# Optimization experiments

Measured on AMD Instinct MI355X. Metric: run time of the kernel, lower is better.

## Reference

```python
import jax, jax.numpy as jnp
import numpy as np

EMBED = 768
NHEAD = 12
HEAD_DIM = EMBED // NHEAD


def setup_inputs() -> dict:
    key = jax.random.key(0)
    ks = jax.random.split(key, 6)
    bs, seq = 4, 2048
    x = jax.random.normal(ks[0], (bs, seq, EMBED), dtype=jnp.float32)
    attmask = jax.random.randint(ks[1], (bs, seq), 0, 2, dtype=jnp.int32)
    # xavier-uniform-ish init for weights
    lim_qkv = float(np.sqrt(6.0 / (EMBED + 3 * EMBED)))
    W_qkv = jax.random.uniform(ks[2], (EMBED, 3 * EMBED), minval=-lim_qkv, maxval=lim_qkv, dtype=jnp.float32)
    b_qkv = jnp.zeros((3 * EMBED,), dtype=jnp.float32)
    lim_p = float(np.sqrt(6.0 / (EMBED + EMBED)))
    W_proj = jax.random.uniform(ks[3], (EMBED, EMBED), minval=-lim_p, maxval=lim_p, dtype=jnp.float32)
    b_proj = jnp.zeros((EMBED,), dtype=jnp.float32)
    return {"x": x, "attmask": attmask, "W_qkv": W_qkv, "b_qkv": b_qkv, "W_proj": W_proj, "b_proj": b_proj}


def reference(x, attmask, W_qkv, b_qkv, W_proj, b_proj):
    bs, seq, embed = x.shape
    qkv = x @ W_qkv + b_qkv                     # [bs, seq, 3*embed]
    q, k, v = jnp.split(qkv, 3, axis=-1)
    def to_heads(t):
        return t.reshape(bs, seq, NHEAD, HEAD_DIM).transpose(0, 2, 1, 3)  # [bs, h, seq, d]
    q, k, v = to_heads(q), to_heads(k), to_heads(v)
    scale = 1.0 / np.sqrt(HEAD_DIM).astype(np.float32)
    scores = jnp.einsum('bhqd,bhkd->bhqk', q, k) * scale  # [bs, h, seq, seq]
    mask = (attmask == 0)[:, None, None, :]               # [bs,1,1,seq]
    scores = jnp.where(mask, jnp.asarray(-10000.0, scores.dtype), scores)
    att = jax.nn.softmax(scores, axis=-1)                  # dropout p=0.0 -> identity
    y = jnp.einsum('bhqk,bhkd->bhqd', att, v)              # [bs, h, seq, d]
    y = y.transpose(0, 2, 1, 3).reshape(bs, seq, embed)
    return y @ W_proj + b_proj
```

## Files before the change

kernel.cpp:

```cpp
#include <hip/hip_runtime.h>

typedef unsigned short u16;
typedef unsigned int u32;
typedef __attribute__((ext_vector_type(8))) short short8;
typedef __attribute__((ext_vector_type(4))) short s16x4;
typedef __attribute__((ext_vector_type(4))) float f32x4;

__device__ __forceinline__ float b2f(u16 u) {
    union { u32 i; float f; } v; v.i = ((u32)u) << 16; return v.f;
}
__device__ __forceinline__ u16 f2b(float f) {
    union { u32 i; float f; } v; v.f = f;
    u32 u = v.i;
    return (u16)((u + 0x7FFFu + ((u >> 16) & 1u)) >> 16);
}
__device__ __forceinline__ f32x4 zero4() {
    f32x4 v; v[0] = 0.f; v[1] = 0.f; v[2] = 0.f; v[3] = 0.f; return v;
}
__device__ __forceinline__ u32 cvtpk(float lo, float hi) {
    u32 d;
    asm("v_cvt_pk_bf16_f32 %0, %1, %2" : "=v"(d) : "v"(lo), "v"(hi));
    return d;
}
__device__ __forceinline__ float fexp2(float x) {
#if __has_builtin(__builtin_amdgcn_exp2f)
    return __builtin_amdgcn_exp2f(x);
#else
    return __expf(x * 0.6931471805599453f);
#endif
}
__device__ __forceinline__ void gload16(const u16* g, u16* l) {
    __builtin_amdgcn_global_load_lds(
        (const __attribute__((address_space(1))) u32*)g,
        (__attribute__((address_space(3))) u32*)l, 16, 0, 0);
}

__device__ __forceinline__ void tconv_body(const float* __restrict__ src,
                                           u16* __restrict__ dst,
                                           int K, int N, int bx, int by) {
    __shared__ u16 T[64][72];
    const int n0 = bx * 64, k0 = by * 64;
    const int tid = threadIdx.x;
    const int r = tid >> 3, cq = tid & 7;
#pragma unroll
    for (int half = 0; half < 2; half++) {
        const int k = k0 + half * 32 + r;
        const float* s = &src[(size_t)k * N + n0 + cq * 8];
        const float4 f0 = ((const float4*)s)[0];
        const float4 f1 = ((const float4*)s)[1];
        T[cq * 8 + 0][half * 32 + r] = f2b(f0.x);
        T[cq * 8 + 1][half * 32 + r] = f2b(f0.y);
        T[cq * 8 + 2][half * 32 + r] = f2b(f0.z);
        T[cq * 8 + 3][half * 32 + r] = f2b(f0.w);
        T[cq * 8 + 4][half * 32 + r] = f2b(f1.x);
        T[cq * 8 + 5][half * 32 + r] = f2b(f1.y);
        T[cq * 8 + 6][half * 32 + r] = f2b(f1.z);
        T[cq * 8 + 7][half * 32 + r] = f2b(f1.w);
    }
    __syncthreads();
#pragma unroll
    for (int half = 0; half < 2; half++) {
        const int n = half * 32 + r;
        short8 o = *(const short8*)&T[n][cq * 8];
        *(short8*)&dst[(size_t)(n0 + n) * K + k0 + cq * 8] = o;
    }
}

__global__ void prep_kernel(const float* __restrict__ x, u16* __restrict__ xb,
                            const float* __restrict__ Wqkv, u16* __restrict__ Wqkvb,
                            const float* __restrict__ Wproj, u16* __restrict__ Wprojb,
                            int n8x) {
    const int blk = blockIdx.x;
    if (blk < 432) {
        tconv_body(Wqkv, Wqkvb, 768, 2304, blk % 36, blk / 36);
    } else if (blk < 576) {
        const int id = blk - 432;
        tconv_body(Wproj, Wprojb, 768, 768, id % 12, id / 12);
    } else {
        const int stride = (1152 - 576) * 256;
        for (int i = (blk - 576) * 256 + threadIdx.x; i < n8x; i += stride) {
            const float* s = x + (size_t)i * 8;
            float4 a = ((const float4*)s)[0];
            float4 b = ((const float4*)s)[1];
            short8 o;
            o[0] = (short)f2b(a.x); o[1] = (short)f2b(a.y);
            o[2] = (short)f2b(a.z); o[3] = (short)f2b(a.w);
            o[4] = (short)f2b(b.x); o[5] = (short)f2b(b.y);
            o[6] = (short)f2b(b.z); o[7] = (short)f2b(b.w);
            ((short8*)xb)[i] = o;
        }
    }
}

template <int MODE>
__global__ __launch_bounds__(256, 2) void gemm_bt_kernel(
    const u16* __restrict__ A, const u16* __restrict__ Bt,
    const float* __restrict__ bias,
    u16* __restrict__ O0, u16* __restrict__ O1, u16* __restrict__ O2,
    float* __restrict__ Of,
    int M, int N, int K)
{
    __shared__ u16 As[128 * 64];
    __shared__ u16 Bs[128 * 64];

    const int tid = threadIdx.x;
    const int nwgx = gridDim.x;
    const int nwg = nwgx * gridDim.y;
    int lin = blockIdx.y * nwgx + blockIdx.x;
    lin = (lin & 7) * (nwg >> 3) + (lin >> 3);
    const int m0 = (lin / nwgx) * 128, n0 = (lin % nwgx) * 128;
    const int lane = tid & 63, w = tid >> 6;
    const int quad = lane >> 4, c = lane & 15;
    const int wm = (w & 1) * 64, wn = (w >> 1) * 64;

    f32x4 acc[4][4];
#pragma unroll
    for (int i = 0; i < 4; i++)
#pragma unroll
        for (int j = 0; j < 4; j++) acc[i][j] = zero4();

    const int srow = lane >> 3;
    const int scol = ((lane & 7) ^ ((srow & 1) << 2)) * 8;
    const size_t abase = (size_t)(m0 + w * 32 + srow) * K + scol;
    const size_t bbase = (size_t)(n0 + w * 32 + srow) * K + scol;
    u16* asl = &As[w * 32 * 64];
    u16* bsl = &Bs[w * 32 * 64];

    const int cpar = (c & 1) << 2;

    for (int k0 = 0; k0 < K; k0 += 64) {
        __syncthreads();
#pragma unroll
        for (int i = 0; i < 4; i++)
            gload16(A + abase + (size_t)(i * 8) * K + k0, asl + i * 512);
#pragma unroll
        for (int i = 0; i < 4; i++)
            gload16(Bt + bbase + (size_t)(i * 8) * K + k0, bsl + i * 512);
        asm volatile("s_waitcnt vmcnt(0)" ::: "memory");
        __syncthreads();

        short8 af[4][2], bfr[4][2];
#pragma unroll
        for (int mi = 0; mi < 4; mi++)
#pragma unroll
            for (int kk = 0; kk < 2; kk++)
                af[mi][kk] = *(const short8*)
                    &As[(wm + mi * 16 + c) * 64 + (((kk * 4 + quad) ^ cpar) * 8)];
#pragma unroll
        for (int ni = 0; ni < 4; ni++)
#pragma unroll
            for (int kk = 0; kk < 2; kk++)
                bfr[ni][kk] = *(const short8*)
                    &Bs[(wn + ni * 16 + c) * 64 + (((kk * 4 + quad) ^ cpar) * 8)];
#pragma unroll
        for (int kk = 0; kk < 2; kk++)
#pragma unroll
            for (int mi = 0; mi < 4; mi++)
#pragma unroll
                for (int ni = 0; ni < 4; ni++)
                    acc[mi][ni] = __builtin_amdgcn_mfma_f32_16x16x32_bf16(
                        af[mi][kk], bfr[ni][kk], acc[mi][ni], 0, 0, 0);
    }

#pragma unroll
    for (int ni = 0; ni < 4; ni++) {
        const int gc = n0 + wn + ni * 16 + c;
        const float bv = bias[gc];
        if (MODE == 0) {
            const int which = gc / 768;
            const int e = gc - which * 768;
            const int hh = e >> 6, d = e & 63;
            u16* op = (which == 0) ? O0 : (which == 1 ? O1 : O2);
#pragma unroll
            for (int mi = 0; mi < 4; mi++)
#pragma unroll
                for (int r = 0; r < 4; r++) {
                    const int gr = m0 + wm + mi * 16 + quad * 4 + r;
                    const int bb = gr >> 11, s = gr & 2047;
                    op[(((size_t)bb * 12 + hh) * 2048 + s) * 64 + d] =
                        f2b(acc[mi][ni][r] + bv);
                }
        } else {
#pragma unroll
            for (int mi = 0; mi < 4; mi++)
#pragma unroll
                for (int r = 0; r < 4; r++) {
                    const int gr = m0 + wm + mi * 16 + quad * 4 + r;
                    Of[(size_t)gr * N + gc] = acc[mi][ni][r] + bv;
                }
        }
    }
}

__global__ __launch_bounds__(256, 3) void attn_kernel(
    const u16* __restrict__ Q, const u16* __restrict__ Kv,
    const u16* __restrict__ Vv, const int* __restrict__ attmask,
    u16* __restrict__ Y)
{
    const int S = 2048, D = 64, NH = 12;
    __shared__ u16 Ks[64][72];
    __shared__ u16 Vs[64][68];
    __shared__ u16 Ps[4][2][16][72];
    __shared__ float msf[2048];

    const int tid = threadIdx.x;
    const int w = tid >> 6, lane = tid & 63;
    const int quad = lane >> 4, c = lane & 15;
    const int bh = blockIdx.x;
    const int qt = blockIdx.y;
    const int b = bh / NH, h = bh - b * NH;

    const u16* Qh = Q + (size_t)bh * S * D;
    const u16* Kh = Kv + (size_t)bh * S * D;
    const u16* Vh = Vv + (size_t)bh * S * D;
    const int q0 = qt * 128 + w * 16;

    short8 aq00 = *(const short8*)&Qh[(size_t)(q0 + c) * D + quad * 8];
    short8 aq01 = *(const short8*)&Qh[(size_t)(q0 + c) * D + 32 + quad * 8];
    short8 aq10 = *(const short8*)&Qh[(size_t)(q0 + 64 + c) * D + quad * 8];
    short8 aq11 = *(const short8*)&Qh[(size_t)(q0 + 64 + c) * D + 32 + quad * 8];

    for (int i = tid; i < S; i += 256)
        msf[i] = (attmask[b * S + i] == 0) ? -43282.0f : 0.0f;

    f32x4 o_acc[2][4];
#pragma unroll
    for (int g = 0; g < 2; g++)
#pragma unroll
        for (int i = 0; i < 4; i++) o_acc[g][i] = zero4();
    float l0 = 0.f, l1 = 0.f;

    const int kpos = tid >> 2, kd = (tid & 3) * 8;
    const int p2 = tid >> 3, vd = (tid & 7) * 8;

    short8 k0r = *(const short8*)&Kh[(size_t)kpos * D + kd];
    short8 k1r = *(const short8*)&Kh[(size_t)kpos * D + kd + 32];
    short8 v0r = *(const short8*)&Vh[(size_t)(2 * p2) * D + vd];
    short8 v1r = *(const short8*)&Vh[(size_t)(2 * p2 + 1) * D + vd];

    const float SC = 0.18033688f;

    for (int kt = 0; kt < S / 64; kt++) {
        asm volatile("" ::: "memory");
        __builtin_amdgcn_s_barrier();
        asm volatile("" ::: "memory");
        *(short8*)&Ks[kpos][kd] = k0r;
        *(short8*)&Ks[kpos][kd + 32] = k1r;
#pragma unroll
        for (int j = 0; j < 8; j++) {
            u32 pk = (u32)(u16)v0r[j] | ((u32)(u16)v1r[j] << 16);
            *(u32*)&Vs[vd + j][2 * p2] = pk;
        }
        if (kt + 1 < S / 64) {
            const int nb = (kt + 1) * 64;
            k0r = *(const short8*)&Kh[(size_t)(nb + kpos) * D + kd];
            k1r = *(const short8*)&Kh[(size_t)(nb + kpos) * D + kd + 32];
            v0r = *(const short8*)&Vh[(size_t)(nb + 2 * p2) * D + vd];
            v1r = *(const short8*)&Vh[(size_t)(nb + 2 * p2 + 1) * D + vd];
        }
        asm volatile("s_waitcnt lgkmcnt(0)" ::: "memory");
        __builtin_amdgcn_s_barrier();
        asm volatile("" ::: "memory");

        const int kbase = kt * 64;

        f32x4 s0[4], s1[4];
#pragma unroll
        for (int ni = 0; ni < 4; ni++) { s0[ni] = zero4(); s1[ni] = zero4(); }
        __builtin_amdgcn_s_setprio(1);
#pragma unroll
        for (int ni = 0; ni < 4; ni++) {
            short8 bk0 = *(const short8*)&Ks[ni * 16 + c][quad * 8];
            short8 bk1 = *(const short8*)&Ks[ni * 16 + c][32 + quad * 8];
            s0[ni] = __builtin_amdgcn_mfma_f32_16x16x32_bf16(bk0, aq00, s0[ni], 0, 0, 0);
            s0[ni] = __builtin_amdgcn_mfma_f32_16x16x32_bf16(bk1, aq01, s0[ni], 0, 0, 0);
            s1[ni] = __builtin_amdgcn_mfma_f32_16x16x32_bf16(bk0, aq10, s1[ni], 0, 0, 0);
            s1[ni] = __builtin_amdgcn_mfma_f32_16x16x32_bf16(bk1, aq11, s1[ni], 0, 0, 0);
        }
        __builtin_amdgcn_s_setprio(0);

#pragma unroll
        for (int ni = 0; ni < 4; ni++) {
            const f32x4 bias = *(const f32x4*)&msf[kbase + ni * 16 + quad * 4];
            {
                float p0 = fexp2(fmaf(s0[ni][0], SC, bias[0]));
                float p1 = fexp2(fmaf(s0[ni][1], SC, bias[1]));
                float p2f = fexp2(fmaf(s0[ni][2], SC, bias[2]));
                float p3 = fexp2(fmaf(s0[ni][3], SC, bias[3]));
                l0 += (p0 + p1) + (p2f + p3);
                uint2 pk;
                pk.x = cvtpk(p0, p1);
                pk.y = cvtpk(p2f, p3);
                *(uint2*)&Ps[w][0][c][ni * 16 + quad * 4] = pk;
            }
            {
                float p0 = fexp2(fmaf(s1[ni][0], SC, bias[0]));
                float p1 = fexp2(fmaf(s1[ni][1], SC, bias[1]));
                float p2f = fexp2(fmaf(s1[ni][2], SC, bias[2]));
                float p3 = fexp2(fmaf(s1[ni][3], SC, bias[3]));
                l1 += (p0 + p1) + (p2f + p3);
                uint2 pk;
                pk.x = cvtpk(p0, p1);
                pk.y = cvtpk(p2f, p3);
                *(uint2*)&Ps[w][1][c][ni * 16 + quad * 4] = pk;
            }
        }

        short8 ap00 = *(const short8*)&Ps[w][0][c][quad * 8];
        short8 ap01 = *(const short8*)&Ps[w][0][c][32 + quad * 8];
        short8 ap10 = *(const short8*)&Ps[w][1][c][quad * 8];
        short8 ap11 = *(const short8*)&Ps[w][1][c][32 + quad * 8];
        __builtin_amdgcn_s_setprio(1);
#pragma unroll
        for (int ni = 0; ni < 4; ni++) {
            union { short8 v8; s16x4 v4[2]; } u0, u1;
            u0.v4[0] = *(const s16x4*)&Vs[ni * 16 + c][quad * 8];
            u0.v4[1] = *(const s16x4*)&Vs[ni * 16 + c][quad * 8 + 4];
            u1.v4[0] = *(const s16x4*)&Vs[ni * 16 + c][32 + quad * 8];
            u1.v4[1] = *(const s16x4*)&Vs[ni * 16 + c][32 + quad * 8 + 4];
            o_acc[0][ni] = __builtin_amdgcn_mfma_f32_16x16x32_bf16(ap00, u0.v8, o_acc[0][ni], 0, 0, 0);
            o_acc[0][ni] = __builtin_amdgcn_mfma_f32_16x16x32_bf16(ap01, u1.v8, o_acc[0][ni], 0, 0, 0);
            o_acc[1][ni] = __builtin_amdgcn_mfma_f32_16x16x32_bf16(ap10, u0.v8, o_acc[1][ni], 0, 0, 0);
            o_acc[1][ni] = __builtin_amdgcn_mfma_f32_16x16x32_bf16(ap11, u1.v8, o_acc[1][ni], 0, 0, 0);
        }
        __builtin_amdgcn_s_setprio(0);
    }

    l0 += __shfl_xor(l0, 16);
    l0 += __shfl_xor(l0, 32);
    l1 += __shfl_xor(l1, 16);
    l1 += __shfl_xor(l1, 32);

    const size_t ybase = ((size_t)b * S) * 768 + h * 64;
#pragma unroll
    for (int r = 0; r < 4; r++) {
        const float lr0 = __shfl(l0, quad * 4 + r);
        const float lr1 = __shfl(l1, quad * 4 + r);
        const float inv0 = 1.f / fmaxf(lr0, 1e-30f);
        const float inv1 = 1.f / fmaxf(lr1, 1e-30f);
        const int srow0 = qt * 128 + w * 16 + quad * 4 + r;
        const int srow1 = srow0 + 64;
#pragma unroll
        for (int ni = 0; ni < 4; ni++) {
            Y[ybase + (size_t)srow0 * 768 + ni * 16 + c] = f2b(o_acc[0][ni][r] * inv0);
            Y[ybase + (size_t)srow1 * 768 + ni * 16 + c] = f2b(o_acc[1][ni][r] * inv1);
        }
    }
}

extern "C" void kernel_launch(void* const* d_in, const int* in_sizes, int n_in,
                              void* d_out, int out_size, void* d_ws, size_t ws_size,
                              hipStream_t stream) {
    const float* x     = (const float*)d_in[0];
    const int* attmask = (const int*)d_in[1];
    const float* Wqkv  = (const float*)d_in[2];
    const float* bqkv  = (const float*)d_in[3];
    const float* Wproj = (const float*)d_in[4];
    const float* bproj = (const float*)d_in[5];
    float* outf = (float*)d_out;

    u16* base = (u16*)d_ws;
    const size_t nx = 4ull * 2048 * 768;
    const size_t nwqkv = 768ull * 2304;
    const size_t nwproj = 768ull * 768;
    u16* xb     = base;
    u16* Wqkvb  = xb + nx;
    u16* Wprojb = Wqkvb + nwqkv;
    u16* Qb     = Wprojb + nwproj;
    const size_t headElems = 48ull * 2048 * 64;
    u16* Kb = Qb + headElems;
    u16* Vb = Kb + headElems;
    u16* Yb = Vb + headElems;

    prep_kernel<<<1152, 256, 0, stream>>>(x, xb, Wqkv, Wqkvb, Wproj, Wprojb,
                                          (int)(nx / 8));

    gemm_bt_kernel<0><<<dim3(18, 64), 256, 0, stream>>>(
        xb, Wqkvb, bqkv, Qb, Kb, Vb, nullptr, 8192, 2304, 768);
    attn_kernel<<<dim3(48, 16), 256, 0, stream>>>(Qb, Kb, Vb, attmask, Yb);
    gemm_bt_kernel<1><<<dim3(6, 64), 256, 0, stream>>>(
        Yb, Wprojb, bproj, nullptr, nullptr, nullptr, outf, 8192, 768, 768);
}
```

Measured before the change: 227.8 us.

## Double-buffer GEMM LDS tiles and vectorize epilogue via swapped MFMA operands

The projection GEMM kernel gets two LDS buffers per operand, so the next K tile is prefetched while MFMAs run on the current one, with a partial vmcnt wait and raw barriers. The MFMA operand order is swapped so each lane holds four consecutive output columns, which lets the epilogue pack bf16 pairs and issue 8-byte (QKV) or 16-byte (fp32) stores with a vector bias load instead of scalar stores. The cost is doubled LDS use, 64 KB per block, which may limit occupancy under launch_bounds(256,2).

```diff
diff --git a/kernel.cpp b/kernel.cpp
--- a/kernel.cpp
+++ b/kernel.cpp
@@ -100,8 +100,8 @@
     float* __restrict__ Of,
     int M, int N, int K)
 {
-    __shared__ u16 As[128 * 64];
-    __shared__ u16 Bs[128 * 64];
+    __shared__ u16 As[2][128 * 64];
+    __shared__ u16 Bs[2][128 * 64];
 
     const int tid = threadIdx.x;
     const int nwgx = gridDim.x;
@@ -123,21 +123,42 @@
     const int scol = ((lane & 7) ^ ((srow & 1) << 2)) * 8;
     const size_t abase = (size_t)(m0 + w * 32 + srow) * K + scol;
     const size_t bbase = (size_t)(n0 + w * 32 + srow) * K + scol;
-    u16* asl = &As[w * 32 * 64];
-    u16* bsl = &Bs[w * 32 * 64];
 
     const int cpar = (c & 1) << 2;
 
-    for (int k0 = 0; k0 < K; k0 += 64) {
-        __syncthreads();
+    {
+        u16* asl = &As[0][w * 2048];
+        u16* bsl = &Bs[0][w * 2048];
 #pragma unroll
         for (int i = 0; i < 4; i++)
-            gload16(A + abase + (size_t)(i * 8) * K + k0, asl + i * 512);
+            gload16(A + abase + (size_t)(i * 8) * K, asl + i * 512);
 #pragma unroll
         for (int i = 0; i < 4; i++)
-            gload16(Bt + bbase + (size_t)(i * 8) * K + k0, bsl + i * 512);
-        asm volatile("s_waitcnt vmcnt(0)" ::: "memory");
-        __syncthreads();
+            gload16(Bt + bbase + (size_t)(i * 8) * K, bsl + i * 512);
+    }
+
+    const int niter = K >> 6;
+    int cur = 0;
+    for (int it = 0; it < niter; it++) {
+        asm volatile("" ::: "memory");
+        __builtin_amdgcn_s_barrier();
+        asm volatile("" ::: "memory");
+        if (it + 1 < niter) {
+            const size_t k1 = (size_t)(it + 1) * 64;
+            u16* asl = &As[cur ^ 1][w * 2048];
+            u16* bsl = &Bs[cur ^ 1][w * 2048];
+#pragma unroll
+            for (int i = 0; i < 4; i++)
+                gload16(A + abase + (size_t)(i * 8) * K + k1, asl + i * 512);
+#pragma unroll
+            for (int i = 0; i < 4; i++)
+                gload16(Bt + bbase + (size_t)(i * 8) * K + k1, bsl + i * 512);
+            asm volatile("s_waitcnt vmcnt(8)" ::: "memory");
+        } else {
+            asm volatile("s_waitcnt vmcnt(0)" ::: "memory");
+        }
+        __builtin_amdgcn_s_barrier();
+        asm volatile("" ::: "memory");
 
         short8 af[4][2], bfr[4][2];
 #pragma unroll
@@ -145,13 +166,13 @@
 #pragma unroll
             for (int kk = 0; kk < 2; kk++)
                 af[mi][kk] = *(const short8*)
-                    &As[(wm + mi * 16 + c) * 64 + (((kk * 4 + quad) ^ cpar) * 8)];
+                    &As[cur][(wm + mi * 16 + c) * 64 + (((kk * 4 + quad) ^ cpar) * 8)];
 #pragma unroll
         for (int ni = 0; ni < 4; ni++)
 #pragma unroll
             for (int kk = 0; kk < 2; kk++)
                 bfr[ni][kk] = *(const short8*)
-                    &Bs[(wn + ni * 16 + c) * 64 + (((kk * 4 + quad) ^ cpar) * 8)];
+                    &Bs[cur][(wn + ni * 16 + c) * 64 + (((kk * 4 + quad) ^ cpar) * 8)];
 #pragma unroll
         for (int kk = 0; kk < 2; kk++)
 #pragma unroll
@@ -159,35 +180,39 @@
 #pragma unroll
                 for (int ni = 0; ni < 4; ni++)
                     acc[mi][ni] = __builtin_amdgcn_mfma_f32_16x16x32_bf16(
-                        af[mi][kk], bfr[ni][kk], acc[mi][ni], 0, 0, 0);
+                        bfr[ni][kk], af[mi][kk], acc[mi][ni], 0, 0, 0);
+        cur ^= 1;
     }
 
 #pragma unroll
     for (int ni = 0; ni < 4; ni++) {
-        const int gc = n0 + wn + ni * 16 + c;
-        const float bv = bias[gc];
+        const int gcb = n0 + wn + ni * 16 + quad * 4;
+        const f32x4 bv = *(const f32x4*)&bias[gcb];
         if (MODE == 0) {
-            const int which = gc / 768;
-            const int e = gc - which * 768;
+            const int which = gcb / 768;
+            const int e = gcb - which * 768;
             const int hh = e >> 6, d = e & 63;
             u16* op = (which == 0) ? O0 : (which == 1 ? O1 : O2);
 #pragma unroll
-            for (int mi = 0; mi < 4; mi++)
-#pragma unroll
-                for (int r = 0; r < 4; r++) {
-                    const int gr = m0 + wm + mi * 16 + quad * 4 + r;
-                    const int bb = gr >> 11, s = gr & 2047;
-                    op[(((size_t)bb * 12 + hh) * 2048 + s) * 64 + d] =
-                        f2b(acc[mi][ni][r] + bv);
-                }
+            for (int mi = 0; mi < 4; mi++) {
+                const int gr = m0 + wm + mi * 16 + c;
+                const int bb = gr >> 11, s = gr & 2047;
+                uint2 pk;
+                pk.x = cvtpk(acc[mi][ni][0] + bv[0], acc[mi][ni][1] + bv[1]);
+                pk.y = cvtpk(acc[mi][ni][2] + bv[2], acc[mi][ni][3] + bv[3]);
+                *(uint2*)&op[(((size_t)bb * 12 + hh) * 2048 + s) * 64 + d] = pk;
+            }
         } else {
 #pragma unroll
-            for (int mi = 0; mi < 4; mi++)
-#pragma unroll
-                for (int r = 0; r < 4; r++) {
-                    const int gr = m0 + wm + mi * 16 + quad * 4 + r;
-                    Of[(size_t)gr * N + gc] = acc[mi][ni][r] + bv;
-                }
+            for (int mi = 0; mi < 4; mi++) {
+                const int gr = m0 + wm + mi * 16 + c;
+                float4 o;
+                o.x = acc[mi][ni][0] + bv[0];
+                o.y = acc[mi][ni][1] + bv[1];
+                o.z = acc[mi][ni][2] + bv[2];
+                o.w = acc[mi][ni][3] + bv[3];
+                *(float4*)&Of[(size_t)gr * N + gcb] = o;
+            }
         }
     }
 }
```

Result: slower. 242.9 us (+6.6%).
